# Performance work log

Measured on AMD Instinct MI355X. Metric: run time of the kernel, lower is better.

The kernel has to match this reference:

```python
import jax, jax.numpy as jnp
import numpy as np

NEG_SLOPE = 0.2

def setup_inputs() -> dict:
    key = jax.random.key(0)
    k1, k2, k3, k4 = jax.random.split(key, 4)
    B, n, d_in, d_out = 8, 2048, 128, 128
    x = jax.random.normal(k1, (B, n, d_in), dtype=jnp.float32)
    adj = jax.random.uniform(k2, (B, n, n), dtype=jnp.float32)
    # glorot init for W: std = sqrt(2/(fan_in+fan_out))
    W = jax.random.normal(k3, (d_in, d_out), dtype=jnp.float32) * np.sqrt(2.0 / (d_in + d_out))
    a = jax.random.normal(k4, (2 * d_out,), dtype=jnp.float32) * np.sqrt(2.0 / (2 * d_out + 1))
    return {"x": x, "adj": adj, "W": W, "a": a}

def reference(x, adj, W, a):
    d_out = W.shape[1]
    h = jnp.einsum('bni,io->bno', x, W)               # [B,n,d_out]
    x_weighted = jnp.einsum('bnm,bmo->bno', adj, h)   # adj @ Wx
    # additive attention: a @ concat(h_i, h_j) == h_i@a_src + h_j@a_dst
    a_src, a_dst = a[:d_out], a[d_out:]
    s_i = h @ a_src                                   # [B,n]
    s_j = h @ a_dst                                   # [B,n]
    e = jax.nn.leaky_relu(s_i[:, :, None] + s_j[:, None, :], NEG_SLOPE)  # [B,n,n]
    alpha = jax.nn.softmax(e, axis=2)
    out = jnp.einsum('bnm,bmo->bno', alpha, h) + x_weighted
    return jax.nn.leaky_relu(out, NEG_SLOPE)
```

## Files before the change

kernel.cpp:

```cpp
#include <hip/hip_runtime.h>
#include <hip/hip_bf16.h>

#define NEG 0.2f
#define LOG2E 1.4426950408889634f

typedef __attribute__((ext_vector_type(8))) short bf16x8;
typedef __attribute__((ext_vector_type(4))) float f32x4;
typedef __attribute__((ext_vector_type(16))) float f32x16;
typedef __attribute__((ext_vector_type(4))) int int4v;

__device__ __forceinline__ float lrelu(float t){ return fmaxf(t, NEG * t); }
__device__ __forceinline__ float fast_exp2(float x){
  float r; asm("v_exp_f32 %0, %1" : "=v"(r) : "v"(x)); return r;
}
__device__ __forceinline__ unsigned short f2bf(float f){
  union { float f; unsigned int u; } v; v.f = f;
  unsigned int r = v.u + 0x7FFFu + ((v.u >> 16) & 1u);
  return (unsigned short)(r >> 16);
}

__global__ __launch_bounds__(256) void k0_wt(const float* __restrict__ W,
                                             unsigned short* __restrict__ Wt){
  __shared__ __align__(16) unsigned short wl[128*136];
  const int t = threadIdx.x;
  {
    const int k = t >> 1, oh = (t & 1) * 64;
#pragma unroll 8
    for (int e = 0; e < 64; ++e)
      wl[(oh + e)*136 + k] = f2bf(W[k*128 + oh + e]);
  }
  __syncthreads();
  {
    const int o = t >> 1, ks = (t & 1) * 64;
#pragma unroll
    for (int g = 0; g < 8; ++g){
      int4v v = *(const int4v*)(wl + o*136 + ks + g*8);
      *(int4v*)(Wt + o*128 + ks + g*8) = v;
    }
  }
}

__global__ __launch_bounds__(256) void k1_fused(const float* __restrict__ x,
                                                const unsigned short* __restrict__ Wt,
                                                const float* __restrict__ a,
                                                unsigned short* __restrict__ ht,
                                                float* __restrict__ ssrcL,
                                                float* __restrict__ sdstL){
  __shared__ __align__(16) unsigned short wtl[128*136];
  __shared__ __align__(16) unsigned short xl[32*136];
  __shared__ __align__(16) unsigned short tlw[128*34];
  __shared__ float sred[2][4][2][16];
  const int t = threadIdx.x;
  const int bx = blockIdx.x;
  const int b  = bx >> 6;
  const int jt = bx & 63;
  const long rowbase = (long)bx * 32;
  {
    const int o = t >> 1, seg = (t & 1) * 64;
    const int4v* src = (const int4v*)(Wt + o*128 + seg);
    int4v* dst = (int4v*)(wtl + o*136 + seg);
#pragma unroll
    for (int g = 0; g < 8; ++g) dst[g] = src[g];
  }
  {
    const int i = t >> 3, ks = (t & 7) * 16;
    const f32x4* src = (const f32x4*)(x + (rowbase + i)*128 + ks);
    unsigned int q[8];
#pragma unroll
    for (int g = 0; g < 4; ++g){
      f32x4 v = src[g];
      q[g*2]   = (unsigned)f2bf(v[0]) | ((unsigned)f2bf(v[1]) << 16);
      q[g*2+1] = (unsigned)f2bf(v[2]) | ((unsigned)f2bf(v[3]) << 16);
    }
    int4v* dst = (int4v*)(xl + i*136 + ks);
    dst[0] = *(int4v*)&q[0];
    dst[1] = *(int4v*)&q[4];
  }
  __syncthreads();
  const int w = t >> 6, lane = t & 63, lr = lane & 15, hi = lane >> 4;
  f32x4 zro = {0.f, 0.f, 0.f, 0.f};
  f32x4 acc00 = zro, acc01 = zro, acc10 = zro, acc11 = zro;
#pragma unroll
  for (int ks = 0; ks < 4; ++ks){
    const bf16x8 a0 = *(const bf16x8*)(wtl + (w*32      + lr)*136 + ks*32 + hi*8);
    const bf16x8 a1 = *(const bf16x8*)(wtl + (w*32 + 16 + lr)*136 + ks*32 + hi*8);
    const bf16x8 b0 = *(const bf16x8*)(xl + (     lr)*136 + ks*32 + hi*8);
    const bf16x8 b1 = *(const bf16x8*)(xl + (16 + lr)*136 + ks*32 + hi*8);
    acc00 = __builtin_amdgcn_mfma_f32_16x16x32_bf16(a0, b0, acc00, 0, 0, 0);
    acc01 = __builtin_amdgcn_mfma_f32_16x16x32_bf16(a0, b1, acc01, 0, 0, 0);
    acc10 = __builtin_amdgcn_mfma_f32_16x16x32_bf16(a1, b0, acc10, 0, 0, 0);
    acc11 = __builtin_amdgcn_mfma_f32_16x16x32_bf16(a1, b1, acc11, 0, 0, 0);
  }
  {
    const f32x4 as0 = *(const f32x4*)(a +       w*32      + hi*4);
    const f32x4 as1 = *(const f32x4*)(a +       w*32 + 16 + hi*4);
    const f32x4 ad0 = *(const f32x4*)(a + 128 + w*32      + hi*4);
    const f32x4 ad1 = *(const f32x4*)(a + 128 + w*32 + 16 + hi*4);
    float ps0, ps1, pd0, pd1;
    {
      f32x4 u = acc00*as0 + acc10*as1;  ps0 = u[0]+u[1]+u[2]+u[3];
      f32x4 v = acc01*as0 + acc11*as1;  ps1 = v[0]+v[1]+v[2]+v[3];
      f32x4 p = acc00*ad0 + acc10*ad1;  pd0 = p[0]+p[1]+p[2]+p[3];
      f32x4 r = acc01*ad0 + acc11*ad1;  pd1 = r[0]+r[1]+r[2]+r[3];
    }
#pragma unroll
    for (int off = 16; off <= 32; off <<= 1){
      ps0 += __shfl_xor(ps0, off); ps1 += __shfl_xor(ps1, off);
      pd0 += __shfl_xor(pd0, off); pd1 += __shfl_xor(pd1, off);
    }
    if (hi == 0){
      sred[0][w][0][lr] = ps0; sred[0][w][1][lr] = ps1;
      sred[1][w][0][lr] = pd0; sred[1][w][1][lr] = pd1;
    }
  }
#pragma unroll
  for (int q = 0; q < 4; ++q){
    tlw[(w*32      + hi*4 + q)*34      + lr] = f2bf(acc00[q]);
    tlw[(w*32      + hi*4 + q)*34 + 16 + lr] = f2bf(acc01[q]);
    tlw[(w*32 + 16 + hi*4 + q)*34      + lr] = f2bf(acc10[q]);
    tlw[(w*32 + 16 + hi*4 + q)*34 + 16 + lr] = f2bf(acc11[q]);
  }
  __syncthreads();
  {
    const int o = t >> 1, jseg = (t & 1) * 16;
    const unsigned int* src = (const unsigned int*)(tlw + o*34 + jseg);
    unsigned int p[8];
#pragma unroll
    for (int g = 0; g < 8; ++g) p[g] = src[g];
    unsigned short* dst = ht + (long)b*262144 + (long)o*2048 + jt*32 + jseg;
    ((int4v*)dst)[0] = *(int4v*)&p[0];
    ((int4v*)dst)[1] = *(int4v*)&p[4];
  }
  if (t < 64){
    const int sel = t >> 5, jl = t & 31;
    const int ig = jl >> 4, l2 = jl & 15;
    const float s = sred[sel][0][ig][l2] + sred[sel][1][ig][l2]
                  + sred[sel][2][ig][l2] + sred[sel][3][ig][l2];
    if (sel == 0) ssrcL[rowbase + jl] = s * LOG2E;
    else          sdstL[rowbase + jl] = s * LOG2E;
  }
}

__global__ __launch_bounds__(256) void k2_ml(const float* __restrict__ ssrcL,
                                             const float* __restrict__ sdstL,
                                             float* __restrict__ carr){
  const int lane = threadIdx.x & 63;
  const long row = (long)blockIdx.x * 4 + (threadIdx.x >> 6);
  const int b = (int)(row >> 11);
  const float siL = ssrcL[row];
  const float* sd = sdstL + (long)b*2048;
  float mx = -3.4e38f;
#pragma unroll
  for (int k = 0; k < 8; ++k){
    f32x4 v = *(const f32x4*)(sd + lane*4 + k*256);
    mx = fmaxf(mx, fmaxf(fmaxf(v[0], v[1]), fmaxf(v[2], v[3])));
  }
#pragma unroll
  for (int off = 1; off <= 32; off <<= 1) mx = fmaxf(mx, __shfl_xor(mx, off));
  const float mL = lrelu(siL + mx);
  float sum = 0.f;
#pragma unroll
  for (int k = 0; k < 8; ++k){
    f32x4 v = *(const f32x4*)(sd + lane*4 + k*256);
#pragma unroll
    for (int e = 0; e < 4; ++e) sum += fast_exp2(lrelu(siL + v[e]) - mL);
  }
#pragma unroll
  for (int off = 1; off <= 32; off <<= 1) sum += __shfl_xor(sum, off);
  if (lane == 0) carr[row] = mL + __log2f(sum);
}

__global__ __launch_bounds__(256, 2) void k3_main(const float* __restrict__ adj,
                                                  const unsigned short* __restrict__ ht,
                                                  const float* __restrict__ ssrcL,
                                                  const float* __restrict__ sdstL,
                                                  const float* __restrict__ carr,
                                                  float* __restrict__ out){
  __shared__ __align__(16) unsigned short httile[2][128][64];
  __shared__ __align__(16) unsigned short wtile[2][32][64];
  const int t    = threadIdx.x;
  const int bxr  = blockIdx.x;
  const int bx   = ((bxr & 7) << 6) | (bxr >> 3);
  const int b    = bx >> 6;
  const int i0   = (bx & 63) * 32;
  const int w    = t >> 6, lane = t & 63;
  const int r32  = lane & 31, hl = lane >> 5;
  const int r7   = r32 & 7;
  const int wchunk = (w*2 + hl) ^ r7;
  const long rowg = (long)b*2048 + i0 + r32;
  const float siL = ssrcL[rowg];
  const float Ci  = carr[rowg];
  const float* adjL = adj + rowg*2048 + w*16 + hl*8;
  const float* sdbL = sdstL + (long)b*2048 + w*16 + hl*8;
  const unsigned short* sgbase = ht + (long)b*262144
                               + (long)(w*32 + (lane >> 3))*2048
                               + ((lane & 7) ^ (lane >> 3)) * 8;

  f32x16 acc;
#pragma unroll
  for (int e = 0; e < 16; ++e) acc[e] = 0.f;
  f32x4 aA0, aA1, dA0, dA1, aB0, aB1, dB0, dB1;

#pragma unroll
  for (int it = 0; it < 4; ++it)
    __builtin_amdgcn_global_load_lds(
      (const __attribute__((address_space(1))) void*)(sgbase + it*16384),
      (__attribute__((address_space(3))) void*)&httile[0][w*32 + it*8][0], 16, 0, 0);
  aA0 = *(const f32x4*)(adjL);      aA1 = *(const f32x4*)(adjL + 4);
  dA0 = *(const f32x4*)(sdbL);      dA1 = *(const f32x4*)(sdbL + 4);
  aB0 = *(const f32x4*)(adjL + 64); aB1 = *(const f32x4*)(adjL + 68);
  dB0 = *(const f32x4*)(sdbL + 64); dB1 = *(const f32x4*)(sdbL + 68);

#define K3_STEP(JB, BUF, DO_STAGE, DO_REFILL, VMSTR, AV0, AV1, DV0, DV1) do{     \
    if (DO_STAGE){                                                               \
      _Pragma("unroll")                                                          \
      for (int it = 0; it < 4; ++it)                                             \
        __builtin_amdgcn_global_load_lds(                                        \
          (const __attribute__((address_space(1))) void*)(sgbase + (JB) + 64 + it*16384), \
          (__attribute__((address_space(3))) void*)&httile[(BUF)^1][w*32 + it*8][0], 16, 0, 0); \
    }                                                                            \
    {  float wv[8];                                                              \
       _Pragma("unroll")                                                         \
       for (int e = 0; e < 4; ++e){                                              \
         wv[e]   = AV0[e] + fast_exp2(lrelu(siL + DV0[e]) - Ci);                 \
         wv[4+e] = AV1[e] + fast_exp2(lrelu(siL + DV1[e]) - Ci);                 \
       }                                                                         \
       const unsigned p01 = __builtin_amdgcn_perm(__float_as_uint(wv[1]), __float_as_uint(wv[0]), 0x07060302u); \
       const unsigned p23 = __builtin_amdgcn_perm(__float_as_uint(wv[3]), __float_as_uint(wv[2]), 0x07060302u); \
       const unsigned p45 = __builtin_amdgcn_perm(__float_as_uint(wv[5]), __float_as_uint(wv[4]), 0x07060302u); \
       const unsigned p67 = __builtin_amdgcn_perm(__float_as_uint(wv[7]), __float_as_uint(wv[6]), 0x07060302u); \
       int4v ai = {(int)p01, (int)p23, (int)p45, (int)p67};                      \
       *(int4v*)&wtile[BUF][r32][wchunk*8] = ai;                                 \
    }                                                                            \
    if (DO_REFILL){                                                              \
      AV0 = *(const f32x4*)(adjL + (JB) + 128);                                  \
      AV1 = *(const f32x4*)(adjL + (JB) + 132);                                  \
      DV0 = *(const f32x4*)(sdbL + (JB) + 128);                                  \
      DV1 = *(const f32x4*)(sdbL + (JB) + 132);                                  \
    }                                                                            \
    asm volatile("s_waitcnt vmcnt(" VMSTR ") lgkmcnt(0)" ::: "memory");          \
    __builtin_amdgcn_sched_barrier(0);                                           \
    __builtin_amdgcn_s_barrier();                                                \
    __builtin_amdgcn_sched_barrier(0);                                           \
    __builtin_amdgcn_s_setprio(1);                                               \
    _Pragma("unroll")                                                            \
    for (int g = 0; g < 4; ++g){                                                 \
      const int pos = ((2*g + hl) ^ r7) * 8;                                     \
      const bf16x8 afr = *(const bf16x8*)&wtile[BUF][r32][pos];                  \
      const bf16x8 bfr = *(const bf16x8*)&httile[BUF][w*32 + r32][pos];          \
      acc = __builtin_amdgcn_mfma_f32_32x32x16_bf16(afr, bfr, acc, 0, 0, 0);     \
    }                                                                            \
    __builtin_amdgcn_s_setprio(0);                                               \
    __builtin_amdgcn_sched_barrier(0);                                           \
  }while(0)

  for (int kt = 0; kt < 30; kt += 2){
    const int jb0 = kt * 64;
    K3_STEP(jb0,      0, 1, 1, "8", aA0, aA1, dA0, dA1);
    K3_STEP(jb0 + 64, 1, 1, 1, "8", aB0, aB1, dB0, dB1);
  }
  K3_STEP(1920, 0, 1, 0, "8", aA0, aA1, dA0, dA1);
  K3_STEP(1984, 1, 0, 0, "0", aB0, aB1, dB0, dB1);
#undef K3_STEP

#pragma unroll
  for (int rg = 0; rg < 16; ++rg){
    const int rr = (rg & 3) + 8*(rg >> 2) + 4*hl;
    out[((long)b*2048 + i0 + rr)*128 + w*32 + r32] = lrelu(acc[rg]);
  }
}

extern "C" void kernel_launch(void* const* d_in, const int* in_sizes, int n_in,
                              void* d_out, int out_size, void* d_ws, size_t ws_size,
                              hipStream_t stream){
  const float* x   = (const float*)d_in[0];
  const float* adj = (const float*)d_in[1];
  const float* W   = (const float*)d_in[2];
  const float* a   = (const float*)d_in[3];
  float* out = (float*)d_out;
  char* ws = (char*)d_ws;

  unsigned short* ht    = (unsigned short*)(ws);
  float*          ssrcL = (float*)(ws + 4194304);
  float*          sdstL = (float*)(ws + 4259840);
  float*          carr  = (float*)(ws + 4325376);
  unsigned short* Wt    = (unsigned short*)(ws + 4390912);

  k0_wt   <<<1,    256, 0, stream>>>(W, Wt);
  k1_fused<<<512,  256, 0, stream>>>(x, Wt, a, ht, ssrcL, sdstL);
  k2_ml   <<<4096, 256, 0, stream>>>(ssrcL, sdstL, carr);
  k3_main <<<512,  256, 0, stream>>>(adj, ht, ssrcL, sdstL, carr, out);
}
```

Baseline: 52.66 us.

## Split k3 K-dimension across two wave groups with 512-thread blocks and precompute row max

The main kernel now uses 512 threads per block, with two groups of four waves each handling half of every 64-wide K tile. Each wave computes half as many adjacency weights per step, and the two partial accumulators are summed through shared memory before the output is written. A separate tiny kernel computes the per-batch max of the destination scores once, so k2_ml no longer recomputes it for every row. The aim is more wave-level parallelism for the memory-bound adj stream. The costs are an extra launch, a shared-memory reduction at the end, and a larger 512-thread block that may limit occupancy.

```diff
diff --git a/kernel.cpp b/kernel.cpp
--- a/kernel.cpp
+++ b/kernel.cpp
@@ -8,6 +8,7 @@
 typedef __attribute__((ext_vector_type(4))) float f32x4;
 typedef __attribute__((ext_vector_type(16))) float f32x16;
 typedef __attribute__((ext_vector_type(4))) int int4v;
+typedef __attribute__((ext_vector_type(2))) int int2v;
 
 __device__ __forceinline__ float lrelu(float t){ return fmaxf(t, NEG * t); }
 __device__ __forceinline__ float fast_exp2(float x){
@@ -141,27 +142,36 @@
   }
 }
 
+__global__ __launch_bounds__(256) void k2_max(const float* __restrict__ sdstL,
+                                              float* __restrict__ M){
+  __shared__ float red[4];
+  const int b = blockIdx.x, t = threadIdx.x;
+  const int lane = t & 63, w = t >> 6;
+  const f32x4* sd = (const f32x4*)(sdstL + (long)b*2048 + t*8);
+  f32x4 v0 = sd[0], v1 = sd[1];
+  float mx = fmaxf(fmaxf(fmaxf(v0[0], v0[1]), fmaxf(v0[2], v0[3])),
+                   fmaxf(fmaxf(v1[0], v1[1]), fmaxf(v1[2], v1[3])));
+#pragma unroll
+  for (int off = 1; off <= 32; off <<= 1) mx = fmaxf(mx, __shfl_xor(mx, off));
+  if (lane == 0) red[w] = mx;
+  __syncthreads();
+  if (t == 0) M[b] = fmaxf(fmaxf(red[0], red[1]), fmaxf(red[2], red[3]));
+}
+
 __global__ __launch_bounds__(256) void k2_ml(const float* __restrict__ ssrcL,
                                              const float* __restrict__ sdstL,
+                                             const float* __restrict__ M,
                                              float* __restrict__ carr){
   const int lane = threadIdx.x & 63;
   const long row = (long)blockIdx.x * 4 + (threadIdx.x >> 6);
   const int b = (int)(row >> 11);
   const float siL = ssrcL[row];
+  const float mL = lrelu(siL + M[b]);
   const float* sd = sdstL + (long)b*2048;
-  float mx = -3.4e38f;
+  float sum = 0.f;
 #pragma unroll
   for (int k = 0; k < 8; ++k){
     f32x4 v = *(const f32x4*)(sd + lane*4 + k*256);
-    mx = fmaxf(mx, fmaxf(fmaxf(v[0], v[1]), fmaxf(v[2], v[3])));
-  }
-#pragma unroll
-  for (int off = 1; off <= 32; off <<= 1) mx = fmaxf(mx, __shfl_xor(mx, off));
-  const float mL = lrelu(siL + mx);
-  float sum = 0.f;
-#pragma unroll
-  for (int k = 0; k < 8; ++k){
-    f32x4 v = *(const f32x4*)(sd + lane*4 + k*256);
 #pragma unroll
     for (int e = 0; e < 4; ++e) sum += fast_exp2(lrelu(siL + v[e]) - mL);
   }
@@ -170,73 +180,67 @@
   if (lane == 0) carr[row] = mL + __log2f(sum);
 }
 
-__global__ __launch_bounds__(256, 2) void k3_main(const float* __restrict__ adj,
+__global__ __launch_bounds__(512, 4) void k3_main(const float* __restrict__ adj,
                                                   const unsigned short* __restrict__ ht,
                                                   const float* __restrict__ ssrcL,
                                                   const float* __restrict__ sdstL,
                                                   const float* __restrict__ carr,
                                                   float* __restrict__ out){
-  __shared__ __align__(16) unsigned short httile[2][128][64];
-  __shared__ __align__(16) unsigned short wtile[2][32][64];
+  __shared__ __align__(16) char smem[40960];
+  unsigned short (*httile)[2][128][32] = (unsigned short (*)[2][128][32])smem;
+  unsigned short (*wtile)[32][64]      = (unsigned short (*)[32][64])(smem + 32768);
+  float* red = (float*)smem;
   const int t    = threadIdx.x;
   const int bxr  = blockIdx.x;
   const int bx   = ((bxr & 7) << 6) | (bxr >> 3);
   const int b    = bx >> 6;
   const int i0   = (bx & 63) * 32;
   const int w    = t >> 6, lane = t & 63;
+  const int cg   = w & 3, sh = w >> 2;
   const int r32  = lane & 31, hl = lane >> 5;
   const int r7   = r32 & 7;
-  const int wchunk = (w*2 + hl) ^ r7;
   const long rowg = (long)b*2048 + i0 + r32;
   const float siL = ssrcL[rowg];
   const float Ci  = carr[rowg];
-  const float* adjL = adj + rowg*2048 + w*16 + hl*8;
-  const float* sdbL = sdstL + (long)b*2048 + w*16 + hl*8;
+  const float* adjL = adj + rowg*2048 + w*8 + hl*4;
+  const float* sdbL = sdstL + (long)b*2048 + w*8 + hl*4;
   const unsigned short* sgbase = ht + (long)b*262144
-                               + (long)(w*32 + (lane >> 3))*2048
-                               + ((lane & 7) ^ (lane >> 3)) * 8;
+                               + (long)(cg*32 + (lane >> 2))*2048 + sh*32
+                               + (((lane & 3) ^ ((lane >> 2) & 3))) * 8;
 
   f32x16 acc;
 #pragma unroll
   for (int e = 0; e < 16; ++e) acc[e] = 0.f;
-  f32x4 aA0, aA1, dA0, dA1, aB0, aB1, dB0, dB1;
-
-#pragma unroll
-  for (int it = 0; it < 4; ++it)
+  f32x4 avA, dvA, avB, dvB;
+
+#pragma unroll
+  for (int rr = 0; rr < 2; ++rr)
     __builtin_amdgcn_global_load_lds(
-      (const __attribute__((address_space(1))) void*)(sgbase + it*16384),
-      (__attribute__((address_space(3))) void*)&httile[0][w*32 + it*8][0], 16, 0, 0);
-  aA0 = *(const f32x4*)(adjL);      aA1 = *(const f32x4*)(adjL + 4);
-  dA0 = *(const f32x4*)(sdbL);      dA1 = *(const f32x4*)(sdbL + 4);
-  aB0 = *(const f32x4*)(adjL + 64); aB1 = *(const f32x4*)(adjL + 68);
-  dB0 = *(const f32x4*)(sdbL + 64); dB1 = *(const f32x4*)(sdbL + 68);
-
-#define K3_STEP(JB, BUF, DO_STAGE, DO_REFILL, VMSTR, AV0, AV1, DV0, DV1) do{     \
+      (const __attribute__((address_space(1))) void*)(sgbase + rr*32768),
+      (__attribute__((address_space(3))) void*)&httile[0][sh][cg*32 + rr*16][0], 16, 0, 0);
+  avA = *(const f32x4*)(adjL);      dvA = *(const f32x4*)(sdbL);
+  avB = *(const f32x4*)(adjL + 64); dvB = *(const f32x4*)(sdbL + 64);
+
+#define K3_STEP(KT, BUF, DO_STAGE, DO_REFILL, VMSTR, AV, DV) do{                 \
     if (DO_STAGE){                                                               \
       _Pragma("unroll")                                                          \
-      for (int it = 0; it < 4; ++it)                                             \
+      for (int rr = 0; rr < 2; ++rr)                                             \
         __builtin_amdgcn_global_load_lds(                                        \
-          (const __attribute__((address_space(1))) void*)(sgbase + (JB) + 64 + it*16384), \
-          (__attribute__((address_space(3))) void*)&httile[(BUF)^1][w*32 + it*8][0], 16, 0, 0); \
+          (const __attribute__((address_space(1))) void*)(sgbase + ((KT)+1)*64 + rr*32768), \
+          (__attribute__((address_space(3))) void*)&httile[(BUF)^1][sh][cg*32 + rr*16][0], 16, 0, 0); \
     }                                                                            \
-    {  float wv[8];                                                              \
+    {  float wv[4];                                                              \
        _Pragma("unroll")                                                         \
-       for (int e = 0; e < 4; ++e){                                              \
-         wv[e]   = AV0[e] + fast_exp2(lrelu(siL + DV0[e]) - Ci);                 \
-         wv[4+e] = AV1[e] + fast_exp2(lrelu(siL + DV1[e]) - Ci);                 \
-       }                                                                         \
+       for (int e = 0; e < 4; ++e)                                               \
+         wv[e] = AV[e] + fast_exp2(lrelu(siL + DV[e]) - Ci);                     \
        const unsigned p01 = __builtin_amdgcn_perm(__float_as_uint(wv[1]), __float_as_uint(wv[0]), 0x07060302u); \
        const unsigned p23 = __builtin_amdgcn_perm(__float_as_uint(wv[3]), __float_as_uint(wv[2]), 0x07060302u); \
-       const unsigned p45 = __builtin_amdgcn_perm(__float_as_uint(wv[5]), __float_as_uint(wv[4]), 0x07060302u); \
-       const unsigned p67 = __builtin_amdgcn_perm(__float_as_uint(wv[7]), __float_as_uint(wv[6]), 0x07060302u); \
-       int4v ai = {(int)p01, (int)p23, (int)p45, (int)p67};                      \
-       *(int4v*)&wtile[BUF][r32][wchunk*8] = ai;                                 \
+       int2v iv = {(int)p01, (int)p23};                                          \
+       *(int2v*)&wtile[BUF][r32][(w ^ r7)*8 + hl*4] = iv;                        \
     }                                                                            \
     if (DO_REFILL){                                                              \
-      AV0 = *(const f32x4*)(adjL + (JB) + 128);                                  \
-      AV1 = *(const f32x4*)(adjL + (JB) + 132);                                  \
-      DV0 = *(const f32x4*)(sdbL + (JB) + 128);                                  \
-      DV1 = *(const f32x4*)(sdbL + (JB) + 132);                                  \
+      AV = *(const f32x4*)(adjL + ((KT)+2)*64);                                  \
+      DV = *(const f32x4*)(sdbL + ((KT)+2)*64);                                  \
     }                                                                            \
     asm volatile("s_waitcnt vmcnt(" VMSTR ") lgkmcnt(0)" ::: "memory");          \
     __builtin_amdgcn_sched_barrier(0);                                           \
@@ -244,10 +248,9 @@
     __builtin_amdgcn_sched_barrier(0);                                           \
     __builtin_amdgcn_s_setprio(1);                                               \
     _Pragma("unroll")                                                            \
-    for (int g = 0; g < 4; ++g){                                                 \
-      const int pos = ((2*g + hl) ^ r7) * 8;                                     \
-      const bf16x8 afr = *(const bf16x8*)&wtile[BUF][r32][pos];                  \
-      const bf16x8 bfr = *(const bf16x8*)&httile[BUF][w*32 + r32][pos];          \
+    for (int g = 0; g < 2; ++g){                                                 \
+      const bf16x8 afr = *(const bf16x8*)&wtile[BUF][r32][((sh*4 + g*2 + hl) ^ r7)*8]; \
+      const bf16x8 bfr = *(const bf16x8*)&httile[BUF][sh][cg*32 + r32][((g*2 + hl) ^ (r32 & 3))*8]; \
       acc = __builtin_amdgcn_mfma_f32_32x32x16_bf16(afr, bfr, acc, 0, 0, 0);     \
     }                                                                            \
     __builtin_amdgcn_s_setprio(0);                                               \
@@ -255,18 +258,28 @@
   }while(0)
 
   for (int kt = 0; kt < 30; kt += 2){
-    const int jb0 = kt * 64;
-    K3_STEP(jb0,      0, 1, 1, "8", aA0, aA1, dA0, dA1);
-    K3_STEP(jb0 + 64, 1, 1, 1, "8", aB0, aB1, dB0, dB1);
-  }
-  K3_STEP(1920, 0, 1, 0, "8", aA0, aA1, dA0, dA1);
-  K3_STEP(1984, 1, 0, 0, "0", aB0, aB1, dB0, dB1);
+    K3_STEP(kt,     0, 1, 1, "4", avA, dvA);
+    K3_STEP(kt + 1, 1, 1, 1, "4", avB, dvB);
+  }
+  K3_STEP(30, 0, 1, 0, "4", avA, dvA);
+  K3_STEP(31, 1, 0, 0, "0", avB, dvB);
 #undef K3_STEP
 
-#pragma unroll
-  for (int rg = 0; rg < 16; ++rg){
-    const int rr = (rg & 3) + 8*(rg >> 2) + 4*hl;
-    out[((long)b*2048 + i0 + rr)*128 + w*32 + r32] = lrelu(acc[rg]);
+  if (sh == 1){
+#pragma unroll
+    for (int rg = 0; rg < 16; ++rg){
+      const int rr = (rg & 3) + 8*(rg >> 2) + 4*hl;
+      red[cg*1024 + rr*32 + r32] = acc[rg];
+    }
+  }
+  __syncthreads();
+  if (sh == 0){
+#pragma unroll
+    for (int rg = 0; rg < 16; ++rg){
+      const int rr = (rg & 3) + 8*(rg >> 2) + 4*hl;
+      const float v = acc[rg] + red[cg*1024 + rr*32 + r32];
+      out[((long)b*2048 + i0 + rr)*128 + cg*32 + r32] = lrelu(v);
+    }
   }
 }
 
@@ -285,9 +298,11 @@
   float*          sdstL = (float*)(ws + 4259840);
   float*          carr  = (float*)(ws + 4325376);
   unsigned short* Wt    = (unsigned short*)(ws + 4390912);
+  float*          M     = (float*)(ws + 4423680);
 
   k0_wt   <<<1,    256, 0, stream>>>(W, Wt);
   k1_fused<<<512,  256, 0, stream>>>(x, Wt, a, ht, ssrcL, sdstL);
-  k2_ml   <<<4096, 256, 0, stream>>>(ssrcL, sdstL, carr);
-  k3_main <<<512,  256, 0, stream>>>(adj, ht, ssrcL, sdstL, carr, out);
-}
+  k2_max  <<<8,    256, 0, stream>>>(sdstL, M);
+  k2_ml   <<<4096, 256, 0, stream>>>(ssrcL, sdstL, M, carr);
+  k3_main <<<512,  512, 0, stream>>>(adj, ht, ssrcL, sdstL, carr, out);
+}
```

Result: slower. 61.05 us (+15.9%).

## Fold W transpose into projection kernel and precompute per-batch max via atomics

Applied to the files above, without the earlier changes.

Removes the separate single-block W-transpose kernel; each projection block now converts and transposes fp32 W into shared memory itself. The per-batch maximum of the destination scores is computed in the projection kernel using an order-preserving float-to-uint mapping and atomicMax, so the softmax-normalizer kernel skips its max pass over 2048 values per row. This trades one launch and a redundant read pass for a memset, scattered 2-byte LDS stores in every block, and global atomics.

```diff
diff --git a/kernel.cpp b/kernel.cpp
--- a/kernel.cpp
+++ b/kernel.cpp
@@ -18,34 +18,21 @@
   unsigned int r = v.u + 0x7FFFu + ((v.u >> 16) & 1u);
   return (unsigned short)(r >> 16);
 }
-
-__global__ __launch_bounds__(256) void k0_wt(const float* __restrict__ W,
-                                             unsigned short* __restrict__ Wt){
-  __shared__ __align__(16) unsigned short wl[128*136];
-  const int t = threadIdx.x;
-  {
-    const int k = t >> 1, oh = (t & 1) * 64;
-#pragma unroll 8
-    for (int e = 0; e < 64; ++e)
-      wl[(oh + e)*136 + k] = f2bf(W[k*128 + oh + e]);
-  }
-  __syncthreads();
-  {
-    const int o = t >> 1, ks = (t & 1) * 64;
-#pragma unroll
-    for (int g = 0; g < 8; ++g){
-      int4v v = *(const int4v*)(wl + o*136 + ks + g*8);
-      *(int4v*)(Wt + o*128 + ks + g*8) = v;
-    }
-  }
+__device__ __forceinline__ unsigned fmap(float f){
+  unsigned u = __float_as_uint(f);
+  return (u & 0x80000000u) ? ~u : (u | 0x80000000u);
+}
+__device__ __forceinline__ float funmap(unsigned u){
+  return (u & 0x80000000u) ? __uint_as_float(u & 0x7FFFFFFFu) : __uint_as_float(~u);
 }
 
 __global__ __launch_bounds__(256) void k1_fused(const float* __restrict__ x,
-                                                const unsigned short* __restrict__ Wt,
+                                                const float* __restrict__ W,
                                                 const float* __restrict__ a,
                                                 unsigned short* __restrict__ ht,
                                                 float* __restrict__ ssrcL,
-                                                float* __restrict__ sdstL){
+                                                float* __restrict__ sdstL,
+                                                unsigned* __restrict__ Mu){
   __shared__ __align__(16) unsigned short wtl[128*136];
   __shared__ __align__(16) unsigned short xl[32*136];
   __shared__ __align__(16) unsigned short tlw[128*34];
@@ -56,11 +43,17 @@
   const int jt = bx & 63;
   const long rowbase = (long)bx * 32;
   {
-    const int o = t >> 1, seg = (t & 1) * 64;
-    const int4v* src = (const int4v*)(Wt + o*128 + seg);
-    int4v* dst = (int4v*)(wtl + o*136 + seg);
-#pragma unroll
-    for (int g = 0; g < 8; ++g) dst[g] = src[g];
+    const int k = t >> 1, seg = t & 1;
+    const f32x4* src = (const f32x4*)(W + k*128 + seg*64);
+#pragma unroll
+    for (int g = 0; g < 16; ++g){
+      f32x4 v = src[g];
+      const int o = seg*64 + g*4;
+      wtl[(o    )*136 + k] = f2bf(v[0]);
+      wtl[(o + 1)*136 + k] = f2bf(v[1]);
+      wtl[(o + 2)*136 + k] = f2bf(v[2]);
+      wtl[(o + 3)*136 + k] = f2bf(v[3]);
+    }
   }
   {
     const int i = t >> 3, ks = (t & 7) * 16;
@@ -134,30 +127,33 @@
   if (t < 64){
     const int sel = t >> 5, jl = t & 31;
     const int ig = jl >> 4, l2 = jl & 15;
-    const float s = sred[sel][0][ig][l2] + sred[sel][1][ig][l2]
-                  + sred[sel][2][ig][l2] + sred[sel][3][ig][l2];
-    if (sel == 0) ssrcL[rowbase + jl] = s * LOG2E;
-    else          sdstL[rowbase + jl] = s * LOG2E;
+    const float s = (sred[sel][0][ig][l2] + sred[sel][1][ig][l2]
+                   + sred[sel][2][ig][l2] + sred[sel][3][ig][l2]) * LOG2E;
+    if (sel == 0){
+      ssrcL[rowbase + jl] = s;
+    } else {
+      sdstL[rowbase + jl] = s;
+      unsigned u = fmap(s);
+#pragma unroll
+      for (int off = 1; off <= 16; off <<= 1){
+        unsigned o2 = (unsigned)__shfl_xor((int)u, off);
+        u = u > o2 ? u : o2;
+      }
+      if (jl == 0) atomicMax(&Mu[b], u);
+    }
   }
 }
 
 __global__ __launch_bounds__(256) void k2_ml(const float* __restrict__ ssrcL,
                                              const float* __restrict__ sdstL,
+                                             const unsigned* __restrict__ Mu,
                                              float* __restrict__ carr){
   const int lane = threadIdx.x & 63;
   const long row = (long)blockIdx.x * 4 + (threadIdx.x >> 6);
   const int b = (int)(row >> 11);
   const float siL = ssrcL[row];
+  const float mL = lrelu(siL + funmap(Mu[b]));
   const float* sd = sdstL + (long)b*2048;
-  float mx = -3.4e38f;
-#pragma unroll
-  for (int k = 0; k < 8; ++k){
-    f32x4 v = *(const f32x4*)(sd + lane*4 + k*256);
-    mx = fmaxf(mx, fmaxf(fmaxf(v[0], v[1]), fmaxf(v[2], v[3])));
-  }
-#pragma unroll
-  for (int off = 1; off <= 32; off <<= 1) mx = fmaxf(mx, __shfl_xor(mx, off));
-  const float mL = lrelu(siL + mx);
   float sum = 0.f;
 #pragma unroll
   for (int k = 0; k < 8; ++k){
@@ -284,10 +280,10 @@
   float*          ssrcL = (float*)(ws + 4194304);
   float*          sdstL = (float*)(ws + 4259840);
   float*          carr  = (float*)(ws + 4325376);
-  unsigned short* Wt    = (unsigned short*)(ws + 4390912);
-
-  k0_wt   <<<1,    256, 0, stream>>>(W, Wt);
-  k1_fused<<<512,  256, 0, stream>>>(x, Wt, a, ht, ssrcL, sdstL);
-  k2_ml   <<<4096, 256, 0, stream>>>(ssrcL, sdstL, carr);
+  unsigned*       Mu    = (unsigned*)(ws + 4390912);
+
+  hipMemsetAsync(Mu, 0, 32, stream);
+  k1_fused<<<512,  256, 0, stream>>>(x, W, a, ht, ssrcL, sdstL, Mu);
+  k2_ml   <<<4096, 256, 0, stream>>>(ssrcL, sdstL, Mu, carr);
   k3_main <<<512,  256, 0, stream>>>(adj, ht, ssrcL, sdstL, carr, out);
 }
```

After: 59.11 us. +12.3%, slower.
